# Kernel tuning notes

Hardware: AMD Instinct MI355X
Metric: run time of the kernel (lower is better)

## Reference

```python
import jax, jax.numpy as jnp
import numpy as np

N_HEAD = 16
NEG = 1e10


def setup_inputs() -> dict:
    key = jax.random.key(0)
    k1, k2, k3 = jax.random.split(key, 3)
    nx = 1024
    B, S = 2, 2048
    x = jax.random.normal(k1, (B, S, nx), dtype=jnp.float32)
    w_attn = jax.random.normal(k2, (nx, 3 * nx), dtype=jnp.float32) * (1.0 / np.sqrt(nx))
    b_attn = jnp.zeros((3 * nx,), dtype=jnp.float32)
    w_proj = jax.random.normal(k3, (nx, nx), dtype=jnp.float32) * (1.0 / np.sqrt(nx))
    b_proj = jnp.zeros((nx,), dtype=jnp.float32)
    return {"x": x, "w_attn": w_attn, "b_attn": b_attn, "w_proj": w_proj, "b_proj": b_proj}


def reference(x, w_attn, b_attn, w_proj, b_proj):
    B, S, nx = x.shape
    d = nx // N_HEAD
    qkv = x @ w_attn + b_attn                      # [B,S,3*nx]
    q, k, v = jnp.split(qkv, 3, axis=-1)
    # split heads: [B,S,nx] -> [B,H,S,d]
    q = q.reshape(B, S, N_HEAD, d).transpose(0, 2, 1, 3)
    k = k.reshape(B, S, N_HEAD, d).transpose(0, 2, 1, 3)
    v = v.reshape(B, S, N_HEAD, d).transpose(0, 2, 1, 3)
    # present: stack of (key stored as [B,H,S,d], value) like torch code
    present = jnp.stack((k, v))                    # [2,B,H,S,d]
    # scores with scale and additive causal mask (GPT-2 style: w*b - 1e10*(1-b))
    w = jnp.einsum('bhqd,bhkd->bhqk', q, k) / jnp.sqrt(jnp.float32(d))
    mask = jnp.tril(jnp.ones((S, S), dtype=w.dtype))[None, None]
    w = w * mask - NEG * (1.0 - mask)
    w = jax.nn.softmax(w, axis=-1)
    a = jnp.einsum('bhqk,bhkd->bhqd', w, v)        # [B,H,S,d]
    a = a.transpose(0, 2, 1, 3).reshape(B, S, nx)  # merge heads
    a = a @ w_proj + b_proj
    return (a, present)
```

## Files before the change

### kernel.cpp

```cpp
#include <hip/hip_runtime.h>
#include <stdint.h>
#include <stddef.h>

#define DEVI __device__ __forceinline__

typedef __bf16 bf16x8 __attribute__((ext_vector_type(8)));
typedef float  f32x4  __attribute__((ext_vector_type(4)));
typedef float  f32x16 __attribute__((ext_vector_type(16)));
typedef unsigned short u16;
typedef uint32_t u32;
typedef u16 u16x8 __attribute__((ext_vector_type(8)));
typedef u16 u16x4 __attribute__((ext_vector_type(4)));
typedef u32 u32x2 __attribute__((ext_vector_type(2)));
typedef u32 u32x4 __attribute__((ext_vector_type(4)));

typedef __attribute__((address_space(1))) void as1_void;
typedef __attribute__((address_space(3))) void as3_void;

static constexpr float SC = 0.18033688011112042f;

DEVI u16 f2bf(float f) {
  uint32_t u = __builtin_bit_cast(uint32_t, f);
  u += 0x7fffu + ((u >> 16) & 1u);
  return (u16)(u >> 16);
}

DEVI void gload_lds16(const void* g, void* l) {
  __builtin_amdgcn_global_load_lds((as1_void*)(void*)g, (as3_void*)l, 16, 0, 0);
}

#if __has_builtin(__builtin_amdgcn_exp2f)
DEVI float fast_exp2(float x) { return __builtin_amdgcn_exp2f(x); }
#else
DEVI float fast_exp2(float x) { return exp2f(x); }
#endif

DEVI u32 cvtpk(float lo, float hi) {
  u32 r;
  asm("v_cvt_pk_bf16_f32 %0, %1, %2" : "=v"(r) : "v"(lo), "v"(hi));
  return r;
}
DEVI void plswap(u32& a, u32& b) {
  asm("v_permlane32_swap_b32 %0, %1" : "+v"(a), "+v"(b));
}

__global__ __launch_bounds__(256) void k_cvt(const float* __restrict__ in,
                                             u16* __restrict__ out, int n) {
  int i = (blockIdx.x * 256 + threadIdx.x) * 4;
  if (i >= n) return;
  const float4 v = *(const float4*)(in + i);
  u16x4 o = { f2bf(v.x), f2bf(v.y), f2bf(v.z), f2bf(v.w) };
  *(u16x4*)(out + i) = o;
}

__global__ __launch_bounds__(256) void k_tcvt(const float* __restrict__ in,
                                              u16* __restrict__ out, int R, int C) {
  __shared__ float tile[32][33];
  const int c0 = blockIdx.x * 32, r0 = blockIdx.y * 32;
  const int tx = threadIdx.x, ty = threadIdx.y;
#pragma unroll
  for (int i = ty; i < 32; i += 8)
    tile[i][tx] = in[(size_t)(r0 + i) * C + (c0 + tx)];
  __syncthreads();
#pragma unroll
  for (int i = ty; i < 32; i += 8)
    out[(size_t)(c0 + i) * R + (r0 + tx)] = f2bf(tile[tx][i]);
}

template <int EPI>
__global__ __launch_bounds__(256) void k_gemm(
    const u16* __restrict__ A, const u16* __restrict__ Bt,
    const float* __restrict__ bias,
    u16* __restrict__ wq, u16* __restrict__ wk, u16* __restrict__ vt,
    float* __restrict__ pk, float* __restrict__ pv, float* __restrict__ of) {
  constexpr int K = 1024;
  __shared__ __align__(16) u16 Ash[128 * 32];
  __shared__ __align__(16) u16 Bsh[128 * 32];
  const int tid = threadIdx.x;
  const int lane = tid & 63, wid = tid >> 6;
  const int wm = wid >> 1, wn = wid & 1;
  const int lr = lane & 15, lg = lane >> 4;
  const int m0 = blockIdx.y * 128, n0 = blockIdx.x * 128;

  const int c = wid * 64 + lane;
  const u16* Ag1 = A + (size_t)(m0 + (c >> 2)) * K + (c & 3) * 8;
  const u16* Ag2 = A + (size_t)(m0 + 64 + (c >> 2)) * K + (c & 3) * 8;
  const u16* Bg1 = Bt + (size_t)(n0 + (c >> 2)) * K + (c & 3) * 8;
  const u16* Bg2 = Bt + (size_t)(n0 + 64 + (c >> 2)) * K + (c & 3) * 8;
  u16* Ad1 = Ash + wid * 512;
  u16* Ad2 = Ash + 2048 + wid * 512;
  u16* Bd1 = Bsh + wid * 512;
  u16* Bd2 = Bsh + 2048 + wid * 512;

  f32x4 acc[4][4];
#pragma unroll
  for (int i = 0; i < 4; ++i)
#pragma unroll
    for (int j = 0; j < 4; ++j) acc[i][j] = (f32x4)0.0f;

  for (int k0 = 0; k0 < K; k0 += 32) {
    gload_lds16(Ag1 + k0, Ad1);
    gload_lds16(Ag2 + k0, Ad2);
    gload_lds16(Bg1 + k0, Bd1);
    gload_lds16(Bg2 + k0, Bd2);
    __syncthreads();
    bf16x8 af[4], bfr[4];
#pragma unroll
    for (int f = 0; f < 4; ++f) {
      af[f]  = *(const bf16x8*)&Ash[(wm * 64 + f * 16 + lr) * 32 + lg * 8];
      bfr[f] = *(const bf16x8*)&Bsh[(wn * 64 + f * 16 + lr) * 32 + lg * 8];
    }
#pragma unroll
    for (int i = 0; i < 4; ++i)
#pragma unroll
      for (int j = 0; j < 4; ++j)
        acc[i][j] = __builtin_amdgcn_mfma_f32_16x16x32_bf16(af[i], bfr[j], acc[i][j], 0, 0, 0);
    __syncthreads();
  }

  if constexpr (EPI == 0) {
#pragma unroll
    for (int j = 0; j < 4; ++j) {
      const int n = n0 + wn * 64 + j * 16 + lr;
      const float bv = bias[n];
      const int sec = n >> 10;
      const int nn = n & 1023;
      const int h = nn >> 6, dd = nn & 63;
#pragma unroll
      for (int i = 0; i < 4; ++i) {
        const int mb = m0 + wm * 64 + i * 16 + lg * 4;
        const int bb = mb >> 11, ss = mb & 2047;
        const size_t ib = (size_t)(bb * 16 + h) * 131072 + (size_t)ss * 64 + dd;
        if (sec == 0) {
#pragma unroll
          for (int r = 0; r < 4; ++r)
            wq[ib + (size_t)r * 64] = f2bf(acc[i][j][r] + bv);
        } else if (sec == 1) {
#pragma unroll
          for (int r = 0; r < 4; ++r) {
            const float v = acc[i][j][r] + bv;
            wk[ib + (size_t)r * 64] = f2bf(v);
            pk[ib + (size_t)r * 64] = v;
          }
        } else {
          u16x4 vv;
#pragma unroll
          for (int r = 0; r < 4; ++r) {
            const float v = acc[i][j][r] + bv;
            pv[ib + (size_t)r * 64] = v;
            vv[r] = f2bf(v);
          }
          *(u16x4*)(vt + ((size_t)(bb * 16 + h) * 64 + dd) * 2048 + ss) = vv;
        }
      }
    }
  } else {
#pragma unroll
    for (int j = 0; j < 4; ++j) {
      const int n = n0 + wn * 64 + j * 16 + lr;
      const float bv = bias[n];
#pragma unroll
      for (int i = 0; i < 4; ++i) {
        const int mb = m0 + wm * 64 + i * 16 + lg * 4;
#pragma unroll
        for (int r = 0; r < 4; ++r)
          of[(size_t)(mb + r) * 1024 + n] = acc[i][j][r] + bv;
      }
    }
  }
}

__global__ __launch_bounds__(256, 1) void k_attn(const u16* __restrict__ Q,
                                                 const u16* __restrict__ Kp,
                                                 const u16* __restrict__ VT,
                                                 u16* __restrict__ AO) {
  const int tid = threadIdx.x;
  const int lane = tid & 63, w = tid >> 6;
  const int l31 = lane & 31, hi = lane >> 5;
  const int bh = blockIdx.x & 31;
  const int qc = blockIdx.x >> 5;
  const int pair = qc * 4 + w;
  const int b = bh >> 4, h = bh & 15;
  const size_t hb = (size_t)bh * (2048 * 64);

  const u16* Kbase = Kp + hb + (size_t)l31 * 64 + hi * 8;
  const u16* Vbase = VT + hb + (size_t)l31 * 2048 + hi * 8;
  const u16* Qbase = Q  + hb + (size_t)l31 * 64 + hi * 8;

  for (int t = 0; t < 2; ++t) {
    const int qt = (t == 0) ? pair : (63 - pair);
    const int qb = qt * 32;
    const int jtmax = qt >> 1;

    bf16x8 qf0 = *(const bf16x8*)(Qbase + (size_t)qb * 64);
    bf16x8 qf1 = *(const bf16x8*)(Qbase + (size_t)qb * 64 + 16);
    bf16x8 qf2 = *(const bf16x8*)(Qbase + (size_t)qb * 64 + 32);
    bf16x8 qf3 = *(const bf16x8*)(Qbase + (size_t)qb * 64 + 48);

    f32x16 o0 = (f32x16)0.0f, o1 = (f32x16)0.0f;
    float mrun = -1e30f, lrun = 0.0f;

    bf16x8 kf[2][4];
#pragma unroll
    for (int s = 0; s < 2; ++s)
#pragma unroll
      for (int c = 0; c < 4; ++c)
        kf[s][c] = *(const bf16x8*)(Kbase + (size_t)(s * 32) * 64 + c * 16);

    for (int jt = 0; jt <= jtmax; ++jt) {
      const bool last = (jt == jtmax);
      bf16x8 vf[2][4];
#pragma unroll
      for (int mt = 0; mt < 2; ++mt)
#pragma unroll
        for (int c = 0; c < 4; ++c)
          vf[mt][c] = *(const bf16x8*)(Vbase + (size_t)(mt * 32) * 2048 + jt * 64 + c * 16);

      f32x16 s0 = (f32x16)0.0f, s1 = (f32x16)0.0f;
      s0 = __builtin_amdgcn_mfma_f32_32x32x16_bf16(kf[0][0], qf0, s0, 0, 0, 0);
      s1 = __builtin_amdgcn_mfma_f32_32x32x16_bf16(kf[1][0], qf0, s1, 0, 0, 0);
      s0 = __builtin_amdgcn_mfma_f32_32x32x16_bf16(kf[0][1], qf1, s0, 0, 0, 0);
      s1 = __builtin_amdgcn_mfma_f32_32x32x16_bf16(kf[1][1], qf1, s1, 0, 0, 0);
      s0 = __builtin_amdgcn_mfma_f32_32x32x16_bf16(kf[0][2], qf2, s0, 0, 0, 0);
      s1 = __builtin_amdgcn_mfma_f32_32x32x16_bf16(kf[1][2], qf2, s1, 0, 0, 0);
      s0 = __builtin_amdgcn_mfma_f32_32x32x16_bf16(kf[0][3], qf3, s0, 0, 0, 0);
      s1 = __builtin_amdgcn_mfma_f32_32x32x16_bf16(kf[1][3], qf3, s1, 0, 0, 0);

      if (!last) {
#pragma unroll
        for (int s = 0; s < 2; ++s)
#pragma unroll
          for (int c = 0; c < 4; ++c)
            kf[s][c] = *(const bf16x8*)(Kbase + (size_t)((jt + 1) * 64 + s * 32) * 64 + c * 16);
      }

      if (last) {
        const int qrel = l31 + (qb - jt * 64);
        const int h4 = hi * 4;
#pragma unroll
        for (int r = 0; r < 16; ++r) {
          const int kp = (r & 3) + ((r >> 2) << 3) + h4;
          s0[r] = (kp <= qrel) ? s0[r] : -1e30f;
          s1[r] = (kp + 32 <= qrel) ? s1[r] : -1e30f;
        }
      }

      float t8[8];
#pragma unroll
      for (int r = 0; r < 8; ++r)
        t8[r] = fmaxf(fmaxf(s0[r], s0[r + 8]), fmaxf(s1[r], s1[r + 8]));
      float tm = fmaxf(fmaxf(fmaxf(t8[0], t8[1]), fmaxf(t8[2], t8[3])),
                       fmaxf(fmaxf(t8[4], t8[5]), fmaxf(t8[6], t8[7])));
      tm = fmaxf(tm, __shfl_xor(tm, 32));
      if (!__all(tm <= mrun)) {
        const float mnew = fmaxf(mrun, tm);
        const float al = fast_exp2((mrun - mnew) * SC);
        mrun = mnew;
        lrun *= al;
#pragma unroll
        for (int r = 0; r < 16; ++r) { o0[r] *= al; o1[r] *= al; }
      }
      const float nb = -mrun * SC;
#pragma unroll
      for (int r = 0; r < 16; ++r) {
        s0[r] = fast_exp2(fmaf(s0[r], SC, nb));
        s1[r] = fast_exp2(fmaf(s1[r], SC, nb));
      }
      float u8[8];
#pragma unroll
      for (int r = 0; r < 8; ++r)
        u8[r] = (s0[r] + s0[r + 8]) + (s1[r] + s1[r + 8]);
      lrun += ((u8[0] + u8[1]) + (u8[2] + u8[3])) + ((u8[4] + u8[5]) + (u8[6] + u8[7]));

      bf16x8 pb0, pb1, pb2, pb3;
#define PACK_CHUNK(sv, bb, dst)                                   \
      {                                                           \
        u32 a0 = cvtpk(sv[bb + 0], sv[bb + 1]);                   \
        u32 a1 = cvtpk(sv[bb + 2], sv[bb + 3]);                   \
        u32 a2 = cvtpk(sv[bb + 4], sv[bb + 5]);                   \
        u32 a3 = cvtpk(sv[bb + 6], sv[bb + 7]);                   \
        plswap(a0, a2);                                           \
        plswap(a1, a3);                                           \
        u32x4 fv = {a0, a1, a2, a3};                              \
        dst = __builtin_bit_cast(bf16x8, fv);                     \
      }
      PACK_CHUNK(s0, 0, pb0)
      PACK_CHUNK(s0, 8, pb1)
      PACK_CHUNK(s1, 0, pb2)
      PACK_CHUNK(s1, 8, pb3)
#undef PACK_CHUNK

      o0 = __builtin_amdgcn_mfma_f32_32x32x16_bf16(vf[0][0], pb0, o0, 0, 0, 0);
      o1 = __builtin_amdgcn_mfma_f32_32x32x16_bf16(vf[1][0], pb0, o1, 0, 0, 0);
      o0 = __builtin_amdgcn_mfma_f32_32x32x16_bf16(vf[0][1], pb1, o0, 0, 0, 0);
      o1 = __builtin_amdgcn_mfma_f32_32x32x16_bf16(vf[1][1], pb1, o1, 0, 0, 0);
      o0 = __builtin_amdgcn_mfma_f32_32x32x16_bf16(vf[0][2], pb2, o0, 0, 0, 0);
      o1 = __builtin_amdgcn_mfma_f32_32x32x16_bf16(vf[1][2], pb2, o1, 0, 0, 0);
      o0 = __builtin_amdgcn_mfma_f32_32x32x16_bf16(vf[0][3], pb3, o0, 0, 0, 0);
      o1 = __builtin_amdgcn_mfma_f32_32x32x16_bf16(vf[1][3], pb3, o1, 0, 0, 0);
    }

    const float lt = lrun + __shfl_xor(lrun, 32);
    const float inv = 1.0f / lt;
    u16* aorow = AO + (size_t)(b * 2048 + qb + l31) * 1024 + h * 64 + hi * 4;
#pragma unroll
    for (int g = 0; g < 4; ++g) {
      u32 w0 = cvtpk(o0[4 * g + 0] * inv, o0[4 * g + 1] * inv);
      u32 w1 = cvtpk(o0[4 * g + 2] * inv, o0[4 * g + 3] * inv);
      u32x2 ww = {w0, w1};
      *(u32x2*)(aorow + g * 8) = ww;
    }
#pragma unroll
    for (int g = 0; g < 4; ++g) {
      u32 w0 = cvtpk(o1[4 * g + 0] * inv, o1[4 * g + 1] * inv);
      u32 w1 = cvtpk(o1[4 * g + 2] * inv, o1[4 * g + 3] * inv);
      u32x2 ww = {w0, w1};
      *(u32x2*)(aorow + 32 + g * 8) = ww;
    }
  }
}

extern "C" void kernel_launch(void* const* d_in, const int* in_sizes, int n_in,
                              void* d_out, int out_size, void* d_ws, size_t ws_size,
                              hipStream_t stream) {
  const float* x      = (const float*)d_in[0];
  const float* w_attn = (const float*)d_in[1];
  const float* b_attn = (const float*)d_in[2];
  const float* w_proj = (const float*)d_in[3];
  const float* b_proj = (const float*)d_in[4];
  float* out = (float*)d_out;

  char* ws = (char*)d_ws;
  u16* x_bf  = (u16*)(ws);
  u16* wat_t = (u16*)(ws + 8388608);
  u16* wpj_t = (u16*)(ws + 14680064);
  u16* q_ws  = (u16*)(ws + 16777216);
  u16* k_ws  = (u16*)(ws + 25165824);
  u16* vT_ws = (u16*)(ws + 33554432);
  u16* a_ws  = (u16*)(ws + 41943040);

  k_cvt<<<4096, 256, 0, stream>>>(x, x_bf, 4194304);
  k_tcvt<<<dim3(96, 32), dim3(32, 8), 0, stream>>>(w_attn, wat_t, 1024, 3072);
  k_tcvt<<<dim3(32, 32), dim3(32, 8), 0, stream>>>(w_proj, wpj_t, 1024, 1024);

  k_gemm<0><<<dim3(24, 32), 256, 0, stream>>>(x_bf, wat_t, b_attn,
                                              q_ws, k_ws, vT_ws,
                                              out + 4194304, out + 8388608, nullptr);

  k_attn<<<dim3(256), 256, 0, stream>>>(q_ws, k_ws, vT_ws, a_ws);

  k_gemm<1><<<dim3(8, 32), 256, 0, stream>>>(a_ws, wpj_t, b_proj,
                                             nullptr, nullptr, nullptr,
                                             nullptr, nullptr, out);
}
```

Baseline: 162.0 us.

## Split attention KV range across wave pairs and merge partial softmax in LDS

Each attention block now handles two query tiles (a short and a long causal tile), with two waves per tile that each take half of the key range. The second wave writes its partial output, max and sum to shared memory, and the first merges them with flash-decoding style rescaling. The grid grows from 256 to 1024 blocks and launch bounds allow 4 blocks per CU, which increases parallelism and shortens the per-wave serial KV loop. In exchange it adds an LDS round trip, a block barrier and a merge step, and half the waves sit idle during the final write.

```diff
diff --git a/kernel.cpp b/kernel.cpp
--- a/kernel.cpp
+++ b/kernel.cpp
@@ -170,153 +170,184 @@
   }
 }
 
-__global__ __launch_bounds__(256, 1) void k_attn(const u16* __restrict__ Q,
+__global__ __launch_bounds__(256, 4) void k_attn(const u16* __restrict__ Q,
                                                  const u16* __restrict__ Kp,
                                                  const u16* __restrict__ VT,
                                                  u16* __restrict__ AO) {
+  __shared__ float Osl[2][32][64];
+  __shared__ float Msl[2][64];
+  __shared__ float Lsl[2][64];
+
   const int tid = threadIdx.x;
   const int lane = tid & 63, w = tid >> 6;
   const int l31 = lane & 31, hi = lane >> 5;
+  const int s = w & 1, ti = w >> 1;
   const int bh = blockIdx.x & 31;
-  const int qc = blockIdx.x >> 5;
-  const int pair = qc * 4 + w;
+  const int pair = blockIdx.x >> 5;
   const int b = bh >> 4, h = bh & 15;
   const size_t hb = (size_t)bh * (2048 * 64);
+
+  const int qt = ti ? (63 - pair) : pair;
+  const int qb = qt * 32;
+  const int T = (qt >> 1) + 1;
+  const int mid = (T + 1) >> 1;
+  const int lo = s ? mid : 0;
+  const int hiB = s ? T : mid;
+  const int jtmax = T - 1;
 
   const u16* Kbase = Kp + hb + (size_t)l31 * 64 + hi * 8;
   const u16* Vbase = VT + hb + (size_t)l31 * 2048 + hi * 8;
   const u16* Qbase = Q  + hb + (size_t)l31 * 64 + hi * 8;
 
-  for (int t = 0; t < 2; ++t) {
-    const int qt = (t == 0) ? pair : (63 - pair);
-    const int qb = qt * 32;
-    const int jtmax = qt >> 1;
-
-    bf16x8 qf0 = *(const bf16x8*)(Qbase + (size_t)qb * 64);
-    bf16x8 qf1 = *(const bf16x8*)(Qbase + (size_t)qb * 64 + 16);
-    bf16x8 qf2 = *(const bf16x8*)(Qbase + (size_t)qb * 64 + 32);
-    bf16x8 qf3 = *(const bf16x8*)(Qbase + (size_t)qb * 64 + 48);
-
-    f32x16 o0 = (f32x16)0.0f, o1 = (f32x16)0.0f;
-    float mrun = -1e30f, lrun = 0.0f;
-
-    bf16x8 kf[2][4];
-#pragma unroll
-    for (int s = 0; s < 2; ++s)
+  const bf16x8 qf0 = *(const bf16x8*)(Qbase + (size_t)qb * 64);
+  const bf16x8 qf1 = *(const bf16x8*)(Qbase + (size_t)qb * 64 + 16);
+  const bf16x8 qf2 = *(const bf16x8*)(Qbase + (size_t)qb * 64 + 32);
+  const bf16x8 qf3 = *(const bf16x8*)(Qbase + (size_t)qb * 64 + 48);
+
+  f32x16 o0 = (f32x16)0.0f, o1 = (f32x16)0.0f;
+  float mrun = -1e30f, lrun = 0.0f;
+
+  bf16x8 kf[2][4];
+#pragma unroll
+  for (int ss = 0; ss < 2; ++ss)
+#pragma unroll
+    for (int c = 0; c < 4; ++c)
+      kf[ss][c] = *(const bf16x8*)(Kbase + (size_t)(lo * 64 + ss * 32) * 64 + c * 16);
+
+  for (int jt = lo; jt < hiB; ++jt) {
+    bf16x8 vf[2][4];
+#pragma unroll
+    for (int mt = 0; mt < 2; ++mt)
 #pragma unroll
       for (int c = 0; c < 4; ++c)
-        kf[s][c] = *(const bf16x8*)(Kbase + (size_t)(s * 32) * 64 + c * 16);
-
-    for (int jt = 0; jt <= jtmax; ++jt) {
-      const bool last = (jt == jtmax);
-      bf16x8 vf[2][4];
-#pragma unroll
-      for (int mt = 0; mt < 2; ++mt)
+        vf[mt][c] = *(const bf16x8*)(Vbase + (size_t)(mt * 32) * 2048 + jt * 64 + c * 16);
+
+    f32x16 s0 = (f32x16)0.0f, s1 = (f32x16)0.0f;
+    s0 = __builtin_amdgcn_mfma_f32_32x32x16_bf16(kf[0][0], qf0, s0, 0, 0, 0);
+    s1 = __builtin_amdgcn_mfma_f32_32x32x16_bf16(kf[1][0], qf0, s1, 0, 0, 0);
+    s0 = __builtin_amdgcn_mfma_f32_32x32x16_bf16(kf[0][1], qf1, s0, 0, 0, 0);
+    s1 = __builtin_amdgcn_mfma_f32_32x32x16_bf16(kf[1][1], qf1, s1, 0, 0, 0);
+    s0 = __builtin_amdgcn_mfma_f32_32x32x16_bf16(kf[0][2], qf2, s0, 0, 0, 0);
+    s1 = __builtin_amdgcn_mfma_f32_32x32x16_bf16(kf[1][2], qf2, s1, 0, 0, 0);
+    s0 = __builtin_amdgcn_mfma_f32_32x32x16_bf16(kf[0][3], qf3, s0, 0, 0, 0);
+    s1 = __builtin_amdgcn_mfma_f32_32x32x16_bf16(kf[1][3], qf3, s1, 0, 0, 0);
+
+    if (jt + 1 < hiB) {
+#pragma unroll
+      for (int ss = 0; ss < 2; ++ss)
 #pragma unroll
         for (int c = 0; c < 4; ++c)
-          vf[mt][c] = *(const bf16x8*)(Vbase + (size_t)(mt * 32) * 2048 + jt * 64 + c * 16);
-
-      f32x16 s0 = (f32x16)0.0f, s1 = (f32x16)0.0f;
-      s0 = __builtin_amdgcn_mfma_f32_32x32x16_bf16(kf[0][0], qf0, s0, 0, 0, 0);
-      s1 = __builtin_amdgcn_mfma_f32_32x32x16_bf16(kf[1][0], qf0, s1, 0, 0, 0);
-      s0 = __builtin_amdgcn_mfma_f32_32x32x16_bf16(kf[0][1], qf1, s0, 0, 0, 0);
-      s1 = __builtin_amdgcn_mfma_f32_32x32x16_bf16(kf[1][1], qf1, s1, 0, 0, 0);
-      s0 = __builtin_amdgcn_mfma_f32_32x32x16_bf16(kf[0][2], qf2, s0, 0, 0, 0);
-      s1 = __builtin_amdgcn_mfma_f32_32x32x16_bf16(kf[1][2], qf2, s1, 0, 0, 0);
-      s0 = __builtin_amdgcn_mfma_f32_32x32x16_bf16(kf[0][3], qf3, s0, 0, 0, 0);
-      s1 = __builtin_amdgcn_mfma_f32_32x32x16_bf16(kf[1][3], qf3, s1, 0, 0, 0);
-
-      if (!last) {
-#pragma unroll
-        for (int s = 0; s < 2; ++s)
-#pragma unroll
-          for (int c = 0; c < 4; ++c)
-            kf[s][c] = *(const bf16x8*)(Kbase + (size_t)((jt + 1) * 64 + s * 32) * 64 + c * 16);
+          kf[ss][c] = *(const bf16x8*)(Kbase + (size_t)((jt + 1) * 64 + ss * 32) * 64 + c * 16);
+    }
+
+    if (jt == jtmax) {
+      const int qrel = l31 + (qb - jtmax * 64);
+      const int h4 = hi * 4;
+#pragma unroll
+      for (int r = 0; r < 16; ++r) {
+        const int kp = (r & 3) + ((r >> 2) << 3) + h4;
+        s0[r] = (kp <= qrel) ? s0[r] : -1e30f;
+        s1[r] = (kp + 32 <= qrel) ? s1[r] : -1e30f;
       }
-
-      if (last) {
-        const int qrel = l31 + (qb - jt * 64);
-        const int h4 = hi * 4;
-#pragma unroll
-        for (int r = 0; r < 16; ++r) {
-          const int kp = (r & 3) + ((r >> 2) << 3) + h4;
-          s0[r] = (kp <= qrel) ? s0[r] : -1e30f;
-          s1[r] = (kp + 32 <= qrel) ? s1[r] : -1e30f;
-        }
-      }
-
-      float t8[8];
-#pragma unroll
-      for (int r = 0; r < 8; ++r)
-        t8[r] = fmaxf(fmaxf(s0[r], s0[r + 8]), fmaxf(s1[r], s1[r + 8]));
-      float tm = fmaxf(fmaxf(fmaxf(t8[0], t8[1]), fmaxf(t8[2], t8[3])),
-                       fmaxf(fmaxf(t8[4], t8[5]), fmaxf(t8[6], t8[7])));
-      tm = fmaxf(tm, __shfl_xor(tm, 32));
-      if (!__all(tm <= mrun)) {
-        const float mnew = fmaxf(mrun, tm);
-        const float al = fast_exp2((mrun - mnew) * SC);
-        mrun = mnew;
-        lrun *= al;
-#pragma unroll
-        for (int r = 0; r < 16; ++r) { o0[r] *= al; o1[r] *= al; }
-      }
-      const float nb = -mrun * SC;
-#pragma unroll
-      for (int r = 0; r < 16; ++r) {
-        s0[r] = fast_exp2(fmaf(s0[r], SC, nb));
-        s1[r] = fast_exp2(fmaf(s1[r], SC, nb));
-      }
-      float u8[8];
-#pragma unroll
-      for (int r = 0; r < 8; ++r)
-        u8[r] = (s0[r] + s0[r + 8]) + (s1[r] + s1[r + 8]);
-      lrun += ((u8[0] + u8[1]) + (u8[2] + u8[3])) + ((u8[4] + u8[5]) + (u8[6] + u8[7]));
-
-      bf16x8 pb0, pb1, pb2, pb3;
+    }
+
+    float t8[8];
+#pragma unroll
+    for (int r = 0; r < 8; ++r)
+      t8[r] = fmaxf(fmaxf(s0[r], s0[r + 8]), fmaxf(s1[r], s1[r + 8]));
+    float tm = fmaxf(fmaxf(fmaxf(t8[0], t8[1]), fmaxf(t8[2], t8[3])),
+                     fmaxf(fmaxf(t8[4], t8[5]), fmaxf(t8[6], t8[7])));
+    tm = fmaxf(tm, __shfl_xor(tm, 32));
+    if (!__all(tm <= mrun)) {
+      const float mnew = fmaxf(mrun, tm);
+      const float al = fast_exp2((mrun - mnew) * SC);
+      mrun = mnew;
+      lrun *= al;
+#pragma unroll
+      for (int r = 0; r < 16; ++r) { o0[r] *= al; o1[r] *= al; }
+    }
+    const float nb = -mrun * SC;
+#pragma unroll
+    for (int r = 0; r < 16; ++r) {
+      s0[r] = fast_exp2(fmaf(s0[r], SC, nb));
+      s1[r] = fast_exp2(fmaf(s1[r], SC, nb));
+    }
+    float u8[8];
+#pragma unroll
+    for (int r = 0; r < 8; ++r)
+      u8[r] = (s0[r] + s0[r + 8]) + (s1[r] + s1[r + 8]);
+    lrun += ((u8[0] + u8[1]) + (u8[2] + u8[3])) + ((u8[4] + u8[5]) + (u8[6] + u8[7]));
+
+    bf16x8 pb0, pb1, pb2, pb3;
 #define PACK_CHUNK(sv, bb, dst)                                   \
-      {                                                           \
-        u32 a0 = cvtpk(sv[bb + 0], sv[bb + 1]);                   \
-        u32 a1 = cvtpk(sv[bb + 2], sv[bb + 3]);                   \
-        u32 a2 = cvtpk(sv[bb + 4], sv[bb + 5]);                   \
-        u32 a3 = cvtpk(sv[bb + 6], sv[bb + 7]);                   \
-        plswap(a0, a2);                                           \
-        plswap(a1, a3);                                           \
-        u32x4 fv = {a0, a1, a2, a3};                              \
-        dst = __builtin_bit_cast(bf16x8, fv);                     \
-      }
-      PACK_CHUNK(s0, 0, pb0)
-      PACK_CHUNK(s0, 8, pb1)
-      PACK_CHUNK(s1, 0, pb2)
-      PACK_CHUNK(s1, 8, pb3)
+    {                                                             \
+      u32 a0 = cvtpk(sv[bb + 0], sv[bb + 1]);                     \
+      u32 a1 = cvtpk(sv[bb + 2], sv[bb + 3]);                     \
+      u32 a2 = cvtpk(sv[bb + 4], sv[bb + 5]);                     \
+      u32 a3 = cvtpk(sv[bb + 6], sv[bb + 7]);                     \
+      plswap(a0, a2);                                             \
+      plswap(a1, a3);                                             \
+      u32x4 fv = {a0, a1, a2, a3};                                \
+      dst = __builtin_bit_cast(bf16x8, fv);                       \
+    }
+    PACK_CHUNK(s0, 0, pb0)
+    PACK_CHUNK(s0, 8, pb1)
+    PACK_CHUNK(s1, 0, pb2)
+    PACK_CHUNK(s1, 8, pb3)
 #undef PACK_CHUNK
 
-      o0 = __builtin_amdgcn_mfma_f32_32x32x16_bf16(vf[0][0], pb0, o0, 0, 0, 0);
-      o1 = __builtin_amdgcn_mfma_f32_32x32x16_bf16(vf[1][0], pb0, o1, 0, 0, 0);
-      o0 = __builtin_amdgcn_mfma_f32_32x32x16_bf16(vf[0][1], pb1, o0, 0, 0, 0);
-      o1 = __builtin_amdgcn_mfma_f32_32x32x16_bf16(vf[1][1], pb1, o1, 0, 0, 0);
-      o0 = __builtin_amdgcn_mfma_f32_32x32x16_bf16(vf[0][2], pb2, o0, 0, 0, 0);
-      o1 = __builtin_amdgcn_mfma_f32_32x32x16_bf16(vf[1][2], pb2, o1, 0, 0, 0);
-      o0 = __builtin_amdgcn_mfma_f32_32x32x16_bf16(vf[0][3], pb3, o0, 0, 0, 0);
-      o1 = __builtin_amdgcn_mfma_f32_32x32x16_bf16(vf[1][3], pb3, o1, 0, 0, 0);
-    }
-
-    const float lt = lrun + __shfl_xor(lrun, 32);
-    const float inv = 1.0f / lt;
-    u16* aorow = AO + (size_t)(b * 2048 + qb + l31) * 1024 + h * 64 + hi * 4;
-#pragma unroll
-    for (int g = 0; g < 4; ++g) {
-      u32 w0 = cvtpk(o0[4 * g + 0] * inv, o0[4 * g + 1] * inv);
-      u32 w1 = cvtpk(o0[4 * g + 2] * inv, o0[4 * g + 3] * inv);
-      u32x2 ww = {w0, w1};
-      *(u32x2*)(aorow + g * 8) = ww;
-    }
-#pragma unroll
-    for (int g = 0; g < 4; ++g) {
-      u32 w0 = cvtpk(o1[4 * g + 0] * inv, o1[4 * g + 1] * inv);
-      u32 w1 = cvtpk(o1[4 * g + 2] * inv, o1[4 * g + 3] * inv);
-      u32x2 ww = {w0, w1};
-      *(u32x2*)(aorow + 32 + g * 8) = ww;
-    }
+    o0 = __builtin_amdgcn_mfma_f32_32x32x16_bf16(vf[0][0], pb0, o0, 0, 0, 0);
+    o1 = __builtin_amdgcn_mfma_f32_32x32x16_bf16(vf[1][0], pb0, o1, 0, 0, 0);
+    o0 = __builtin_amdgcn_mfma_f32_32x32x16_bf16(vf[0][1], pb1, o0, 0, 0, 0);
+    o1 = __builtin_amdgcn_mfma_f32_32x32x16_bf16(vf[1][1], pb1, o1, 0, 0, 0);
+    o0 = __builtin_amdgcn_mfma_f32_32x32x16_bf16(vf[0][2], pb2, o0, 0, 0, 0);
+    o1 = __builtin_amdgcn_mfma_f32_32x32x16_bf16(vf[1][2], pb2, o1, 0, 0, 0);
+    o0 = __builtin_amdgcn_mfma_f32_32x32x16_bf16(vf[0][3], pb3, o0, 0, 0, 0);
+    o1 = __builtin_amdgcn_mfma_f32_32x32x16_bf16(vf[1][3], pb3, o1, 0, 0, 0);
+  }
+
+  if (s) {
+#pragma unroll
+    for (int r = 0; r < 16; ++r) {
+      Osl[ti][r][lane]      = o0[r];
+      Osl[ti][16 + r][lane] = o1[r];
+    }
+    Msl[ti][lane] = mrun;
+    Lsl[ti][lane] = lrun;
+  }
+  __syncthreads();
+  if (s) return;
+
+  {
+    const float mB = Msl[ti][lane];
+    const float lB = Lsl[ti][lane];
+    const float m  = fmaxf(mrun, mB);
+    const float al = fast_exp2((mrun - m) * SC);
+    const float bt = fast_exp2((mB - m) * SC);
+    lrun = lrun * al + lB * bt;
+#pragma unroll
+    for (int r = 0; r < 16; ++r) {
+      o0[r] = o0[r] * al + Osl[ti][r][lane] * bt;
+      o1[r] = o1[r] * al + Osl[ti][16 + r][lane] * bt;
+    }
+  }
+
+  const float lt = lrun + __shfl_xor(lrun, 32);
+  const float inv = 1.0f / lt;
+  u16* aorow = AO + (size_t)(b * 2048 + qb + l31) * 1024 + h * 64 + hi * 4;
+#pragma unroll
+  for (int g = 0; g < 4; ++g) {
+    u32 w0 = cvtpk(o0[4 * g + 0] * inv, o0[4 * g + 1] * inv);
+    u32 w1 = cvtpk(o0[4 * g + 2] * inv, o0[4 * g + 3] * inv);
+    u32x2 ww = {w0, w1};
+    *(u32x2*)(aorow + g * 8) = ww;
+  }
+#pragma unroll
+  for (int g = 0; g < 4; ++g) {
+    u32 w0 = cvtpk(o1[4 * g + 0] * inv, o1[4 * g + 1] * inv);
+    u32 w1 = cvtpk(o1[4 * g + 2] * inv, o1[4 * g + 3] * inv);
+    u32x2 ww = {w0, w1};
+    *(u32x2*)(aorow + 32 + g * 8) = ww;
   }
 }
 
@@ -347,7 +378,7 @@
                                               q_ws, k_ws, vT_ws,
                                               out + 4194304, out + 8388608, nullptr);
 
-  k_attn<<<dim3(256), 256, 0, stream>>>(q_ws, k_ws, vT_ws, a_ws);
+  k_attn<<<dim3(1024), 256, 0, stream>>>(q_ws, k_ws, vT_ws, a_ws);
 
   k_gemm<1><<<dim3(8, 32), 256, 0, stream>>>(a_ws, wpj_t, b_proj,
                                              nullptr, nullptr, nullptr,
```

Result: slower. 232.3 us (+43.4%).

## Double-buffer GEMM LDS tiles and stage attention K/V through swizzled shared memory

Applied to the files above, without the earlier changes.

The GEMM now double-buffers its A/B LDS tiles, so the next k-slice is loaded while MFMAs run on the current one, with a single barrier per step. The attention kernel is restructured: each block handles 128 query rows with four waves sharing K/V tiles, which are staged into double-buffered, XOR-swizzled LDS instead of being loaded per wave from global memory. It launches 512 blocks in a heavy-first order and raises MFMA priority around the matrix ops. In exchange it adds a block-wide barrier per KV step, so waves past their diagonal sit idle while others finish, and LDS use is higher.

```diff
diff --git a/kernel.cpp b/kernel.cpp
--- a/kernel.cpp
+++ b/kernel.cpp
@@ -74,8 +74,8 @@
     u16* __restrict__ wq, u16* __restrict__ wk, u16* __restrict__ vt,
     float* __restrict__ pk, float* __restrict__ pv, float* __restrict__ of) {
   constexpr int K = 1024;
-  __shared__ __align__(16) u16 Ash[128 * 32];
-  __shared__ __align__(16) u16 Bsh[128 * 32];
+  __shared__ __align__(16) u16 Ash[2][128 * 32];
+  __shared__ __align__(16) u16 Bsh[2][128 * 32];
   const int tid = threadIdx.x;
   const int lane = tid & 63, wid = tid >> 6;
   const int wm = wid >> 1, wn = wid & 1;
@@ -87,10 +87,6 @@
   const u16* Ag2 = A + (size_t)(m0 + 64 + (c >> 2)) * K + (c & 3) * 8;
   const u16* Bg1 = Bt + (size_t)(n0 + (c >> 2)) * K + (c & 3) * 8;
   const u16* Bg2 = Bt + (size_t)(n0 + 64 + (c >> 2)) * K + (c & 3) * 8;
-  u16* Ad1 = Ash + wid * 512;
-  u16* Ad2 = Ash + 2048 + wid * 512;
-  u16* Bd1 = Bsh + wid * 512;
-  u16* Bd2 = Bsh + 2048 + wid * 512;
 
   f32x4 acc[4][4];
 #pragma unroll
@@ -98,17 +94,24 @@
 #pragma unroll
     for (int j = 0; j < 4; ++j) acc[i][j] = (f32x4)0.0f;
 
+#define STAGE(sel, kk)                                        \
+  {                                                           \
+    gload_lds16(Ag1 + (kk), &Ash[sel][wid * 512]);            \
+    gload_lds16(Ag2 + (kk), &Ash[sel][2048 + wid * 512]);     \
+    gload_lds16(Bg1 + (kk), &Bsh[sel][wid * 512]);            \
+    gload_lds16(Bg2 + (kk), &Bsh[sel][2048 + wid * 512]);     \
+  }
+
+  STAGE(0, 0)
+  __syncthreads();
+  int cur = 0;
   for (int k0 = 0; k0 < K; k0 += 32) {
-    gload_lds16(Ag1 + k0, Ad1);
-    gload_lds16(Ag2 + k0, Ad2);
-    gload_lds16(Bg1 + k0, Bd1);
-    gload_lds16(Bg2 + k0, Bd2);
-    __syncthreads();
+    if (k0 + 32 < K) STAGE(cur ^ 1, k0 + 32)
     bf16x8 af[4], bfr[4];
 #pragma unroll
     for (int f = 0; f < 4; ++f) {
-      af[f]  = *(const bf16x8*)&Ash[(wm * 64 + f * 16 + lr) * 32 + lg * 8];
-      bfr[f] = *(const bf16x8*)&Bsh[(wn * 64 + f * 16 + lr) * 32 + lg * 8];
+      af[f]  = *(const bf16x8*)&Ash[cur][(wm * 64 + f * 16 + lr) * 32 + lg * 8];
+      bfr[f] = *(const bf16x8*)&Bsh[cur][(wn * 64 + f * 16 + lr) * 32 + lg * 8];
     }
 #pragma unroll
     for (int i = 0; i < 4; ++i)
@@ -116,7 +119,9 @@
       for (int j = 0; j < 4; ++j)
         acc[i][j] = __builtin_amdgcn_mfma_f32_16x16x32_bf16(af[i], bfr[j], acc[i][j], 0, 0, 0);
     __syncthreads();
-  }
+    cur ^= 1;
+  }
+#undef STAGE
 
   if constexpr (EPI == 0) {
 #pragma unroll
@@ -170,53 +175,67 @@
   }
 }
 
-__global__ __launch_bounds__(256, 1) void k_attn(const u16* __restrict__ Q,
-                                                 const u16* __restrict__ Kp,
-                                                 const u16* __restrict__ VT,
-                                                 u16* __restrict__ AO) {
+__global__ __launch_bounds__(256) void k_attn(const u16* __restrict__ Q,
+                                              const u16* __restrict__ Kp,
+                                              const u16* __restrict__ VT,
+                                              u16* __restrict__ AO) {
+  __shared__ __align__(16) u16 Ksh[2][4096];
+  __shared__ __align__(16) u16 Vsh[2][4096];
+
   const int tid = threadIdx.x;
   const int lane = tid & 63, w = tid >> 6;
   const int l31 = lane & 31, hi = lane >> 5;
-  const int bh = blockIdx.x & 31;
-  const int qc = blockIdx.x >> 5;
-  const int pair = qc * 4 + w;
+  const int bid = blockIdx.x;
+  const int bh = bid & 31;
+  const int sb = (bid < 256) ? (15 - (bid >> 5)) : ((bid - 256) >> 5);
   const int b = bh >> 4, h = bh & 15;
   const size_t hb = (size_t)bh * (2048 * 64);
 
-  const u16* Kbase = Kp + hb + (size_t)l31 * 64 + hi * 8;
-  const u16* Vbase = VT + hb + (size_t)l31 * 2048 + hi * 8;
-  const u16* Qbase = Q  + hb + (size_t)l31 * 64 + hi * 8;
-
-  for (int t = 0; t < 2; ++t) {
-    const int qt = (t == 0) ? pair : (63 - pair);
-    const int qb = qt * 32;
-    const int jtmax = qt >> 1;
-
-    bf16x8 qf0 = *(const bf16x8*)(Qbase + (size_t)qb * 64);
-    bf16x8 qf1 = *(const bf16x8*)(Qbase + (size_t)qb * 64 + 16);
-    bf16x8 qf2 = *(const bf16x8*)(Qbase + (size_t)qb * 64 + 32);
-    bf16x8 qf3 = *(const bf16x8*)(Qbase + (size_t)qb * 64 + 48);
-
-    f32x16 o0 = (f32x16)0.0f, o1 = (f32x16)0.0f;
-    float mrun = -1e30f, lrun = 0.0f;
-
-    bf16x8 kf[2][4];
-#pragma unroll
-    for (int s = 0; s < 2; ++s)
-#pragma unroll
-      for (int c = 0; c < 4; ++c)
-        kf[s][c] = *(const bf16x8*)(Kbase + (size_t)(s * 32) * 64 + c * 16);
-
-    for (int jt = 0; jt <= jtmax; ++jt) {
-      const bool last = (jt == jtmax);
-      bf16x8 vf[2][4];
-#pragma unroll
-      for (int mt = 0; mt < 2; ++mt)
+  const int T = 2 * sb + 2;
+  const int qb = sb * 128 + w * 32;
+  const int diag = (qb + 31) >> 6;
+
+  const int srow = w * 16 + (lane >> 3);
+  const int sslot = (lane & 7) ^ ((lane >> 3) & 7);
+  const u16* Kg = Kp + hb + (size_t)srow * 64 + sslot * 8;
+  const u16* Vg = VT + hb + (size_t)srow * 2048 + sslot * 8;
+
+#define STAGEA(sel, jt)                                                   \
+  {                                                                       \
+    gload_lds16(Kg + (size_t)(jt) * 4096,         &Ksh[sel][w * 1024]);   \
+    gload_lds16(Kg + (size_t)(jt) * 4096 + 512,   &Ksh[sel][w * 1024 + 512]); \
+    gload_lds16(Vg + (size_t)(jt) * 64,           &Vsh[sel][w * 1024]);   \
+    gload_lds16(Vg + (size_t)(jt) * 64 + 16384,   &Vsh[sel][w * 1024 + 512]); \
+  }
+
+  const u16* Qp = Q + hb + (size_t)(qb + l31) * 64 + hi * 8;
+  const bf16x8 qf0 = *(const bf16x8*)(Qp);
+  const bf16x8 qf1 = *(const bf16x8*)(Qp + 16);
+  const bf16x8 qf2 = *(const bf16x8*)(Qp + 32);
+  const bf16x8 qf3 = *(const bf16x8*)(Qp + 48);
+
+  f32x16 o0 = (f32x16)0.0f, o1 = (f32x16)0.0f;
+  float mrun = -1e30f, lrun = 0.0f;
+
+  const int xr = l31 & 7;
+
+  STAGEA(0, 0)
+  __syncthreads();
+  int sel = 0;
+  for (int jt = 0; jt < T; ++jt) {
+    if (jt + 1 < T) STAGEA(sel ^ 1, jt + 1)
+    if (jt <= diag) {
+      const u16* Kb = Ksh[sel];
+      const u16* Vb = Vsh[sel];
+      bf16x8 kf[2][4];
+#pragma unroll
+      for (int s = 0; s < 2; ++s)
 #pragma unroll
         for (int c = 0; c < 4; ++c)
-          vf[mt][c] = *(const bf16x8*)(Vbase + (size_t)(mt * 32) * 2048 + jt * 64 + c * 16);
+          kf[s][c] = *(const bf16x8*)&Kb[(s * 32 + l31) * 64 + (((2 * c + hi) ^ xr) * 8)];
 
       f32x16 s0 = (f32x16)0.0f, s1 = (f32x16)0.0f;
+      __builtin_amdgcn_s_setprio(1);
       s0 = __builtin_amdgcn_mfma_f32_32x32x16_bf16(kf[0][0], qf0, s0, 0, 0, 0);
       s1 = __builtin_amdgcn_mfma_f32_32x32x16_bf16(kf[1][0], qf0, s1, 0, 0, 0);
       s0 = __builtin_amdgcn_mfma_f32_32x32x16_bf16(kf[0][1], qf1, s0, 0, 0, 0);
@@ -225,17 +244,10 @@
       s1 = __builtin_amdgcn_mfma_f32_32x32x16_bf16(kf[1][2], qf2, s1, 0, 0, 0);
       s0 = __builtin_amdgcn_mfma_f32_32x32x16_bf16(kf[0][3], qf3, s0, 0, 0, 0);
       s1 = __builtin_amdgcn_mfma_f32_32x32x16_bf16(kf[1][3], qf3, s1, 0, 0, 0);
-
-      if (!last) {
-#pragma unroll
-        for (int s = 0; s < 2; ++s)
-#pragma unroll
-          for (int c = 0; c < 4; ++c)
-            kf[s][c] = *(const bf16x8*)(Kbase + (size_t)((jt + 1) * 64 + s * 32) * 64 + c * 16);
-      }
-
-      if (last) {
-        const int qrel = l31 + (qb - jt * 64);
+      __builtin_amdgcn_s_setprio(0);
+
+      if (jt == diag) {
+        const int qrel = qb + l31 - diag * 64;
         const int h4 = hi * 4;
 #pragma unroll
         for (int r = 0; r < 16; ++r) {
@@ -290,6 +302,14 @@
       PACK_CHUNK(s1, 8, pb3)
 #undef PACK_CHUNK
 
+      bf16x8 vf[2][4];
+#pragma unroll
+      for (int mt = 0; mt < 2; ++mt)
+#pragma unroll
+        for (int c = 0; c < 4; ++c)
+          vf[mt][c] = *(const bf16x8*)&Vb[(mt * 32 + l31) * 64 + (((2 * c + hi) ^ xr) * 8)];
+
+      __builtin_amdgcn_s_setprio(1);
       o0 = __builtin_amdgcn_mfma_f32_32x32x16_bf16(vf[0][0], pb0, o0, 0, 0, 0);
       o1 = __builtin_amdgcn_mfma_f32_32x32x16_bf16(vf[1][0], pb0, o1, 0, 0, 0);
       o0 = __builtin_amdgcn_mfma_f32_32x32x16_bf16(vf[0][1], pb1, o0, 0, 0, 0);
@@ -298,25 +318,29 @@
       o1 = __builtin_amdgcn_mfma_f32_32x32x16_bf16(vf[1][2], pb2, o1, 0, 0, 0);
       o0 = __builtin_amdgcn_mfma_f32_32x32x16_bf16(vf[0][3], pb3, o0, 0, 0, 0);
       o1 = __builtin_amdgcn_mfma_f32_32x32x16_bf16(vf[1][3], pb3, o1, 0, 0, 0);
+      __builtin_amdgcn_s_setprio(0);
     }
-
-    const float lt = lrun + __shfl_xor(lrun, 32);
-    const float inv = 1.0f / lt;
-    u16* aorow = AO + (size_t)(b * 2048 + qb + l31) * 1024 + h * 64 + hi * 4;
-#pragma unroll
-    for (int g = 0; g < 4; ++g) {
-      u32 w0 = cvtpk(o0[4 * g + 0] * inv, o0[4 * g + 1] * inv);
-      u32 w1 = cvtpk(o0[4 * g + 2] * inv, o0[4 * g + 3] * inv);
-      u32x2 ww = {w0, w1};
-      *(u32x2*)(aorow + g * 8) = ww;
-    }
-#pragma unroll
-    for (int g = 0; g < 4; ++g) {
-      u32 w0 = cvtpk(o1[4 * g + 0] * inv, o1[4 * g + 1] * inv);
-      u32 w1 = cvtpk(o1[4 * g + 2] * inv, o1[4 * g + 3] * inv);
-      u32x2 ww = {w0, w1};
-      *(u32x2*)(aorow + 32 + g * 8) = ww;
-    }
+    __syncthreads();
+    sel ^= 1;
+  }
+#undef STAGEA
+
+  const float lt = lrun + __shfl_xor(lrun, 32);
+  const float inv = 1.0f / lt;
+  u16* aorow = AO + (size_t)(b * 2048 + qb + l31) * 1024 + h * 64 + hi * 4;
+#pragma unroll
+  for (int g = 0; g < 4; ++g) {
+    u32 w0 = cvtpk(o0[4 * g + 0] * inv, o0[4 * g + 1] * inv);
+    u32 w1 = cvtpk(o0[4 * g + 2] * inv, o0[4 * g + 3] * inv);
+    u32x2 ww = {w0, w1};
+    *(u32x2*)(aorow + g * 8) = ww;
+  }
+#pragma unroll
+  for (int g = 0; g < 4; ++g) {
+    u32 w0 = cvtpk(o1[4 * g + 0] * inv, o1[4 * g + 1] * inv);
+    u32 w1 = cvtpk(o1[4 * g + 2] * inv, o1[4 * g + 3] * inv);
+    u32x2 ww = {w0, w1};
+    *(u32x2*)(aorow + 32 + g * 8) = ww;
   }
 }
 
@@ -347,7 +371,7 @@
                                               q_ws, k_ws, vT_ws,
                                               out + 4194304, out + 8388608, nullptr);
 
-  k_attn<<<dim3(256), 256, 0, stream>>>(q_ws, k_ws, vT_ws, a_ws);
+  k_attn<<<dim3(512), 256, 0, stream>>>(q_ws, k_ws, vT_ws, a_ws);
 
   k_gemm<1><<<dim3(8, 32), 256, 0, stream>>>(a_ws, wpj_t, b_proj,
                                              nullptr, nullptr, nullptr,
```

After: 135.7 us. -16.3%, faster.
